# Optimization experiments

Hardware: AMD Instinct MI355X
Metric: run time of the kernel (lower is better)

The kernel has to match this reference:

```python
import jax, jax.numpy as jnp
import numpy as np

B, T, F = 4096, 72, 9
H = 64            # GRU units per direction
DENSE = 128
P = 24            # predict_window


def _gru_scan(xp, h0, U, br, act):
    """xp: (T,B,3H) precomputed input projections; Keras reset_after=True GRU."""
    def step(h, x_t):
        rec = h @ U + br                      # (B,3H)
        xz, xr, xh = jnp.split(x_t, 3, axis=-1)
        rz, rr, rh = jnp.split(rec, 3, axis=-1)
        z = jax.nn.sigmoid(xz + rz)
        r = jax.nn.sigmoid(xr + rr)
        hh = act(xh + r * rh)
        h_new = z * h + (1.0 - z) * hh
        return h_new, h_new
    hT, hs = jax.lax.scan(step, h0, xp)
    return hT, hs


def _bigru(x, h0f, h0b, Wf, Uf, bif, brf, Wb, Ub, bib, brb, act, return_sequences):
    xt = jnp.swapaxes(x, 0, 1)                # (T,B,F)
    xpf = xt @ Wf + bif                       # (T,B,3H)
    xpb = xt[::-1] @ Wb + bib                 # reversed time for backward dir
    hTf, hsf = _gru_scan(xpf, h0f, Uf, brf, act)
    hTb, hsb = _gru_scan(xpb, h0b, Ub, brb, act)
    if return_sequences:
        out = jnp.concatenate([hsf, hsb[::-1]], axis=-1)   # (T,B,2H)
        return jnp.swapaxes(out, 0, 1)                      # (B,T,2H)
    return jnp.concatenate([hTf, hTb], axis=-1)             # (B,2H)


def _glorot(key, shape):
    fan_in, fan_out = shape[0], shape[-1]
    lim = np.sqrt(6.0 / (fan_in + fan_out))
    return jax.random.uniform(key, shape, jnp.float32, -lim, lim)


def setup_inputs() -> dict:
    key = jax.random.key(0)
    ks = jax.random.split(key, 16)
    d = {
        "x": jax.random.normal(ks[0], (B, T, F), jnp.float32),
        "h0_fwd": jnp.zeros((B, H), jnp.float32),
        "h0_bwd": jnp.zeros((B, H), jnp.float32),
        # d1 (input F=9), forward & backward directions
        "d1f_W": _glorot(ks[1], (F, 3 * H)), "d1f_U": _glorot(ks[2], (H, 3 * H)),
        "d1f_bi": jnp.zeros((3 * H,), jnp.float32), "d1f_br": jnp.zeros((3 * H,), jnp.float32),
        "d1b_W": _glorot(ks[3], (F, 3 * H)), "d1b_U": _glorot(ks[4], (H, 3 * H)),
        "d1b_bi": jnp.zeros((3 * H,), jnp.float32), "d1b_br": jnp.zeros((3 * H,), jnp.float32),
        # d2 (input 2H=128)
        "d2f_W": _glorot(ks[5], (2 * H, 3 * H)), "d2f_U": _glorot(ks[6], (H, 3 * H)),
        "d2f_bi": jnp.zeros((3 * H,), jnp.float32), "d2f_br": jnp.zeros((3 * H,), jnp.float32),
        "d2b_W": _glorot(ks[7], (2 * H, 3 * H)), "d2b_U": _glorot(ks[8], (H, 3 * H)),
        "d2b_bi": jnp.zeros((3 * H,), jnp.float32), "d2b_br": jnp.zeros((3 * H,), jnp.float32),
        # dense heads
        "dense_W": _glorot(ks[9], (2 * H, DENSE)), "dense_b": jnp.zeros((DENSE,), jnp.float32),
        "out_W": _glorot(ks[10], (DENSE, P)), "out_b": jnp.zeros((P,), jnp.float32),
    }
    return d


def reference(x, h0_fwd, h0_bwd,
              d1f_W, d1f_U, d1f_bi, d1f_br, d1b_W, d1b_U, d1b_bi, d1b_br,
              d2f_W, d2f_U, d2f_bi, d2f_br, d2b_W, d2b_U, d2b_bi, d2b_br,
              dense_W, dense_b, out_W, out_b):
    # d1: Bidirectional GRU(64, activation=relu), return_sequences=True, initial_state=hidden
    seq = _bigru(x, h0_fwd, h0_bwd,
                 d1f_W, d1f_U, d1f_bi, d1f_br,
                 d1b_W, d1b_U, d1b_bi, d1b_br,
                 jax.nn.relu, True)                         # (B,T,128)
    # d2: Bidirectional GRU(64, activation=tanh), zero initial state, last-state output
    z0 = jnp.zeros((x.shape[0], H), seq.dtype)
    feat = _bigru(seq, z0, z0,
                  d2f_W, d2f_U, d2f_bi, d2f_br,
                  d2b_W, d2b_U, d2b_bi, d2b_br,
                  jnp.tanh, False)                          # (B,128)
    h = jax.nn.relu(feat @ dense_W + dense_b)               # (B,128)
    out = jax.nn.softmax(h @ out_W + out_b, axis=-1)        # (B,P)
    return out
```

## Files before the change

kernel.cpp:

```cpp
#include <hip/hip_runtime.h>
#include <hip/hip_bf16.h>

typedef __attribute__((ext_vector_type(8))) short short8;
typedef __attribute__((ext_vector_type(4))) float f32x4;
typedef float float4a __attribute__((ext_vector_type(4), aligned(4)));
typedef unsigned short ushort4u __attribute__((ext_vector_type(4), aligned(2)));
typedef unsigned short ush;

#define MFMA_B16(a, b, c) __builtin_amdgcn_mfma_f32_16x16x32_bf16((a), (b), (c), 0, 0, 0)

__device__ __forceinline__ float bf2f(ush u) {
    union { unsigned int i; float f; } v; v.i = ((unsigned int)u) << 16; return v.f;
}
__device__ __forceinline__ ush f2bf(float f) {
    union { float f; unsigned int i; } v; v.f = f;
    unsigned int r = v.i + 0x7fffu + ((v.i >> 16) & 1u);
    return (ush)(r >> 16);
}
__device__ __forceinline__ float rcp_f(float x) { return __builtin_amdgcn_rcpf(x); }
__device__ __forceinline__ float sigm_pre(float x) {
    return rcp_f(1.0f + __builtin_amdgcn_exp2f(x));
}
__device__ __forceinline__ float tanh_pre(float x) {
    return 1.0f - 2.0f * rcp_f(__builtin_amdgcn_exp2f(x) + 1.0f);
}

__device__ __forceinline__ void lds_barrier() {
    asm volatile("s_waitcnt lgkmcnt(0)" ::: "memory");
    __builtin_amdgcn_s_barrier();
    asm volatile("" ::: "memory");
}

__device__ __forceinline__ bool probe_bf16(const ush* p, int tid, int* s_cnt) {
    if (tid == 0) *s_cnt = 0;
    __syncthreads();
    ush s = p[tid & 255];
    int e = (s >> 7) & 0xFF;
    if (tid < 256 && e >= 117 && e <= 137) atomicAdd(s_cnt, 1);
    __syncthreads();
    return *s_cnt >= 200;
}

struct WArgs {
    const void* src[20];
    int off[21];
};

__global__ __launch_bounds__(256)
void convert_w(WArgs a, ush* __restrict__ arena, const ush* __restrict__ probe)
{
    __shared__ int cnt;
    const bool bf = probe_bf16(probe, threadIdx.x, &cnt);
    const int total = a.off[20];
    for (int i = blockIdx.x * 256 + threadIdx.x; i < total; i += gridDim.x * 256) {
        int t = 0;
        while (t < 19 && i >= a.off[t + 1]) ++t;
        const int local = i - a.off[t];
        float v = bf ? bf2f(((const ush*)a.src[t])[local])
                     : ((const float*)a.src[t])[local];
        if (t < 16) {
            const int col = local % 192;
            if (col < 128) v *= -1.4426950408889634f;
            else if (t >= 8) v *= 2.885390081777927f;
        }
        arena[i] = f2bf(v);
    }
}

struct XR { float4a f; ushort4u h; };

__device__ __forceinline__ XR loadx(const void* X, bool xbf, size_t row72, int tx, int q) {
    XR r;
    r.f = (float4a){0.f, 0.f, 0.f, 0.f};
    r.h = (ushort4u){0, 0, 0, 0};
    if (xbf) {
        const ush* p = (const ush*)X + (row72 + (size_t)tx) * 9 + q * 4;
        if (q < 2) r.h = *(const ushort4u*)p;
        else if (q == 2) r.h[0] = p[0];
    } else {
        const float* p = (const float*)X + (row72 + (size_t)tx) * 9 + q * 4;
        if (q < 2) r.f = *(const float4a*)p;
        else if (q == 2) r.f[0] = p[0];
    }
    return r;
}

__device__ __forceinline__ short8 convx(bool xbf, float4a rf, ushort4u rh) {
    short8 r;
    if (xbf) {
#pragma unroll
        for (int j = 0; j < 4; ++j) { r[2 * j] = (short)rh[j]; r[2 * j + 1] = 0; }
    } else {
#pragma unroll
        for (int j = 0; j < 4; ++j) {
            ush hi = f2bf(rf[j]);
            ush lo = f2bf(rf[j] - bf2f(hi));
            r[2 * j] = (short)hi; r[2 * j + 1] = (short)lo;
        }
    }
    return r;
}

__global__ __launch_bounds__(256, 1)
void gru1_kernel(const void* __restrict__ X, const void* __restrict__ h0f,
                 const void* __restrict__ h0b, int cb, int bchunk,
                 const ush* __restrict__ Wf, const ush* __restrict__ Uf,
                 const ush* __restrict__ bif, const ush* __restrict__ brf,
                 const ush* __restrict__ Wb, const ush* __restrict__ Ub,
                 const ush* __restrict__ bib, const ush* __restrict__ brb,
                 ush* __restrict__ seq)
{
    const int tid  = threadIdx.x;
    const int lane = tid & 63;
    const int wv   = tid >> 6;
    const int q    = lane >> 4;
    const int ln   = lane & 15;
    const int dir  = blockIdx.y;
    const int lb0  = blockIdx.x * 16;
    const int gb0  = cb + lb0;
    const int u    = wv * 16 + ln;

    const ush* W  = dir ? Wb  : Wf;
    const ush* U  = dir ? Ub  : Uf;
    const ush* bi = dir ? bib : bif;
    const ush* br = dir ? brb : brf;
    const void* h0 = dir ? h0b : h0f;

    __shared__ __align__(16) ush Ah[2][16][72];
    __shared__ int s_cnt;

    const bool xbf = probe_bf16((const ush*)X, tid, &s_cnt);

    short8 bU[3][2];
    short8 bW[3];
#pragma unroll
    for (int g = 0; g < 3; ++g) {
        const int col = g * 64 + u;
#pragma unroll
        for (int ks = 0; ks < 2; ++ks) {
            short8 f;
#pragma unroll
            for (int j = 0; j < 8; ++j) {
                int kp = ks * 32 + q * 8 + j;
                f[j] = (short)U[(size_t)kp * 192 + col];
            }
            bU[g][ks] = f;
        }
        short8 fw;
#pragma unroll
        for (int j = 0; j < 8; ++j) {
            int kp = q * 8 + j;
            fw[j] = (kp < 18) ? (short)W[(size_t)(kp >> 1) * 192 + col] : (short)0;
        }
        bW[g] = fw;
    }

    const float bz  = bf2f(bi[u])       + bf2f(br[u]);
    const float brg = bf2f(bi[64 + u])  + bf2f(br[64 + u]);
    const float bih = bf2f(bi[128 + u]);
    const float brh = bf2f(br[128 + u]);
    const f32x4 Cz  = {bz,  bz,  bz,  bz};
    const f32x4 Cr  = {brg, brg, brg, brg};
    const f32x4 Chx = {bih, bih, bih, bih};
    const f32x4 Chr = {brh, brh, brh, brh};

    float hreg[4];
#pragma unroll
    for (int i = 0; i < 4; ++i) {
        int m = q * 4 + i;
        size_t idx = (size_t)(gb0 + m) * 64 + u;
        float hv = xbf ? bf2f(((const ush*)h0)[idx])
                       : ((const float*)h0)[idx];
        hreg[i] = hv;
        Ah[0][m][u] = f2bf(hv);
    }

    const int r2 = tid >> 3, c2 = tid & 7;

    const size_t row72 = (size_t)(gb0 + ln) * 72;
    short8 axc;
    XR rn;
    {
        XR r0 = loadx(X, xbf, row72, dir ? 71 : 0, q);
        axc = convx(xbf, r0.f, r0.h);
        rn  = loadx(X, xbf, row72, dir ? 70 : 1, q);
    }
    __syncthreads();

#pragma unroll 2
    for (int t = 0; t < 72; ++t) {
        const int cur = t & 1, nb = cur ^ 1;

        XR rr;
        rr.f = (float4a){0.f, 0.f, 0.f, 0.f};
        rr.h = (ushort4u){0, 0, 0, 0};
        if (t < 70) rr = loadx(X, xbf, row72, dir ? 69 - t : t + 2, q);

        if (t > 0 && tid < 128) {
            const int tw = dir ? (71 - (t - 1)) : (t - 1);
            int4 v = *(const int4*)&Ah[cur][r2][c2 * 8];
            *(int4*)(seq + ((size_t)tw * bchunk + lb0 + r2) * 128 + dir * 64 + c2 * 8) = v;
        }

        const ush* ap = &Ah[cur][ln][0];
        short8 a0 = *(const short8*)(ap + q * 8);
        short8 a1 = *(const short8*)(ap + 32 + q * 8);
        f32x4 az  = MFMA_B16(axc, bW[0], Cz);
        az        = MFMA_B16(a0, bU[0][0], az);
        az        = MFMA_B16(a1, bU[0][1], az);
        f32x4 ar  = MFMA_B16(axc, bW[1], Cr);
        ar        = MFMA_B16(a0, bU[1][0], ar);
        ar        = MFMA_B16(a1, bU[1][1], ar);
        f32x4 ahx = MFMA_B16(axc, bW[2], Chx);
        f32x4 ahr = MFMA_B16(a0, bU[2][0], Chr);
        ahr       = MFMA_B16(a1, bU[2][1], ahr);

#pragma unroll
        for (int i = 0; i < 4; ++i) {
            const int m = q * 4 + i;
            float z = sigm_pre(az[i]);
            float r = sigm_pre(ar[i]);
            float pre = ahx[i] + r * ahr[i];
            float hh = fmaxf(pre, 0.0f);
            float hn = hh + z * (hreg[i] - hh);
            hreg[i] = hn;
            Ah[nb][m][u] = f2bf(hn);
        }

        axc = convx(xbf, rn.f, rn.h);
        rn = rr;
        lds_barrier();
    }

    if (tid < 128) {
        const int tw = dir ? 0 : 71;
        int4 v = *(const int4*)&Ah[0][r2][c2 * 8];
        *(int4*)(seq + ((size_t)tw * bchunk + lb0 + r2) * 128 + dir * 64 + c2 * 8) = v;
    }
}

__global__ __launch_bounds__(256, 1)
void gru2_kernel(const ush* __restrict__ seq, int cb, int bchunk,
                 const ush* __restrict__ W2f, const ush* __restrict__ U2f,
                 const ush* __restrict__ bi2f, const ush* __restrict__ br2f,
                 const ush* __restrict__ W2b, const ush* __restrict__ U2b,
                 const ush* __restrict__ bi2b, const ush* __restrict__ br2b,
                 float* __restrict__ feat)
{
    const int tid  = threadIdx.x;
    const int lane = tid & 63;
    const int wv   = tid >> 6;
    const int q    = lane >> 4;
    const int ln   = lane & 15;
    const int dir  = blockIdx.y;
    const int lb0  = blockIdx.x * 16;
    const int gb0  = cb + lb0;
    const int u    = wv * 16 + ln;

    const ush* W  = dir ? W2b  : W2f;
    const ush* U  = dir ? U2b  : U2f;
    const ush* bi = dir ? bi2b : bi2f;
    const ush* br = dir ? br2b : br2f;

    __shared__ __align__(16) ush Ah[2][16][72];

    {
        ush* p = &Ah[0][0][0];
        for (int i = tid; i < 16 * 72; i += 256) p[i] = 0;
    }

    const long long tstride = (long long)bchunk * 128 * (dir ? -1 : 1);
    const ush* sptr0 = seq + ((size_t)(lb0 + ln)) * 128 + q * 8
                     + (dir ? 71ll * bchunk * 128 : 0);

    short8 bU[3][2];
    short8 bV[3][4];
#pragma unroll
    for (int g = 0; g < 3; ++g) {
        const int col = g * 64 + u;
#pragma unroll
        for (int ks = 0; ks < 2; ++ks) {
            short8 f;
#pragma unroll
            for (int j = 0; j < 8; ++j) {
                int kp = ks * 32 + q * 8 + j;
                f[j] = (short)U[(size_t)kp * 192 + col];
            }
            bU[g][ks] = f;
        }
#pragma unroll
        for (int ks = 0; ks < 4; ++ks) {
            short8 fv;
#pragma unroll
            for (int j = 0; j < 8; ++j) {
                int kp = ks * 32 + q * 8 + j;
                fv[j] = (short)W[(size_t)kp * 192 + col];
            }
            bV[g][ks] = fv;
        }
    }

    const float bz  = bf2f(bi[u])       + bf2f(br[u]);
    const float brg = bf2f(bi[64 + u])  + bf2f(br[64 + u]);
    const float bih = bf2f(bi[128 + u]);
    const float brh = bf2f(br[128 + u]);
    const f32x4 Cz  = {bz,  bz,  bz,  bz};
    const f32x4 Cr  = {brg, brg, brg, brg};
    const f32x4 Chx = {bih, bih, bih, bih};
    const f32x4 Chr = {brh, brh, brh, brh};

    float hreg[4];
#pragma unroll
    for (int i = 0; i < 4; ++i) hreg[i] = 0.0f;

    f32x4 P0, P1, P2;
    {
        const ush* sp = sptr0;
        short8 s0 = *(const short8*)(sp);
        short8 s1 = *(const short8*)(sp + 32);
        short8 s2 = *(const short8*)(sp + 64);
        short8 s3 = *(const short8*)(sp + 96);
        P0 = MFMA_B16(s0, bV[0][0], Cz);
        P0 = MFMA_B16(s1, bV[0][1], P0);
        P0 = MFMA_B16(s2, bV[0][2], P0);
        P0 = MFMA_B16(s3, bV[0][3], P0);
        P1 = MFMA_B16(s0, bV[1][0], Cr);
        P1 = MFMA_B16(s1, bV[1][1], P1);
        P1 = MFMA_B16(s2, bV[1][2], P1);
        P1 = MFMA_B16(s3, bV[1][3], P1);
        P2 = MFMA_B16(s0, bV[2][0], Chx);
        P2 = MFMA_B16(s1, bV[2][1], P2);
        P2 = MFMA_B16(s2, bV[2][2], P2);
        P2 = MFMA_B16(s3, bV[2][3], P2);
    }
    short8 c0, c1, c2, c3, g0, g1, g2, g3;
    {
        const ush* sp = sptr0 + tstride;
        c0 = *(const short8*)(sp);
        c1 = *(const short8*)(sp + 32);
        c2 = *(const short8*)(sp + 64);
        c3 = *(const short8*)(sp + 96);
    }
    {
        const ush* sp = sptr0 + 2 * tstride;
        g0 = *(const short8*)(sp);
        g1 = *(const short8*)(sp + 32);
        g2 = *(const short8*)(sp + 64);
        g3 = *(const short8*)(sp + 96);
    }
    __syncthreads();

#pragma unroll 2
    for (int t = 0; t < 72; ++t) {
        const int cur = t & 1, nb = cur ^ 1;

        short8 f0 = g0, f1 = g1, f2 = g2, f3 = g3;
        if (t < 69) {
            const ush* sp = sptr0 + (long long)(t + 3) * tstride;
            f0 = *(const short8*)(sp);
            f1 = *(const short8*)(sp + 32);
            f2 = *(const short8*)(sp + 64);
            f3 = *(const short8*)(sp + 96);
        }

        const ush* ap = &Ah[cur][ln][0];
        short8 a0 = *(const short8*)(ap + q * 8);
        short8 a1 = *(const short8*)(ap + 32 + q * 8);
        f32x4 az  = MFMA_B16(a0, bU[0][0], P0);
        az        = MFMA_B16(a1, bU[0][1], az);
        f32x4 ar  = MFMA_B16(a0, bU[1][0], P1);
        ar        = MFMA_B16(a1, bU[1][1], ar);
        f32x4 ahr = MFMA_B16(a0, bU[2][0], Chr);
        ahr       = MFMA_B16(a1, bU[2][1], ahr);
        f32x4 ahx = P2;

#pragma unroll
        for (int i = 0; i < 4; ++i) {
            const int m = q * 4 + i;
            float z = sigm_pre(az[i]);
            float r = sigm_pre(ar[i]);
            float pre = ahx[i] + r * ahr[i];
            float hh = tanh_pre(pre);
            float hn = hh + z * (hreg[i] - hh);
            hreg[i] = hn;
            Ah[nb][m][u] = f2bf(hn);
        }

        if (t < 71) {
            P0 = MFMA_B16(c0, bV[0][0], Cz);
            P0 = MFMA_B16(c1, bV[0][1], P0);
            P0 = MFMA_B16(c2, bV[0][2], P0);
            P0 = MFMA_B16(c3, bV[0][3], P0);
            P1 = MFMA_B16(c0, bV[1][0], Cr);
            P1 = MFMA_B16(c1, bV[1][1], P1);
            P1 = MFMA_B16(c2, bV[1][2], P1);
            P1 = MFMA_B16(c3, bV[1][3], P1);
            P2 = MFMA_B16(c0, bV[2][0], Chx);
            P2 = MFMA_B16(c1, bV[2][1], P2);
            P2 = MFMA_B16(c2, bV[2][2], P2);
            P2 = MFMA_B16(c3, bV[2][3], P2);
        }
        c0 = g0; c1 = g1; c2 = g2; c3 = g3;
        g0 = f0; g1 = f1; g2 = f2; g3 = f3;
        lds_barrier();
    }

#pragma unroll
    for (int i = 0; i < 4; ++i) {
        const int m = q * 4 + i;
        feat[(size_t)(gb0 + m) * 128 + dir * 64 + u] = hreg[i];
    }
}

__global__ __launch_bounds__(256, 1)
void head_kernel(const float* __restrict__ feat,
                 const ush* __restrict__ dW, const ush* __restrict__ db,
                 const ush* __restrict__ oW, const ush* __restrict__ ob,
                 float* __restrict__ out)
{
    const int tid = threadIdx.x;
    const int b0  = blockIdx.x * 16;

    __shared__ __align__(16) ush Wl[128][136];
    __shared__ __align__(16) float fs[16][128];
    __shared__ __align__(16) float hs[16][136];
    __shared__ __align__(16) float ls[16][32];

    for (int i = tid; i < 2048; i += 256) {
        const int k = i >> 4;
        const int c = (i & 15) * 8;
        *(int4*)&Wl[k][c] = *(const int4*)(dW + (size_t)k * 128 + c);
    }
    {
        const float4* src = (const float4*)(feat + (size_t)b0 * 128);
        float4* dst = (float4*)&fs[0][0];
        for (int i = tid; i < 512; i += 256) dst[i] = src[i];
    }
    __syncthreads();

    {
        const int row = tid >> 4;
        const int j0  = (tid & 15) * 8;
        float acc[8];
#pragma unroll
        for (int jj = 0; jj < 8; ++jj) acc[jj] = bf2f(db[j0 + jj]);
        for (int k = 0; k < 128; ++k) {
            float f = fs[row][k];
            short8 w = *(const short8*)&Wl[k][j0];
#pragma unroll
            for (int jj = 0; jj < 8; ++jj)
                acc[jj] += f * bf2f((ush)w[jj]);
        }
#pragma unroll
        for (int jj = 0; jj < 8; ++jj) hs[row][j0 + jj] = fmaxf(acc[jj], 0.0f);
    }
    __syncthreads();

    for (int e = tid; e < 16 * 24; e += 256) {
        const int row = e / 24, l = e - 24 * row;
        float acc = bf2f(ob[l]);
        for (int k = 0; k < 128; ++k)
            acc += hs[row][k] * bf2f(oW[(size_t)k * 24 + l]);
        ls[row][l] = acc;
    }
    __syncthreads();

    for (int e = tid; e < 16 * 24; e += 256) {
        const int row = e / 24, l = e - 24 * row;
        float mx = ls[row][0];
#pragma unroll
        for (int k = 1; k < 24; ++k) mx = fmaxf(mx, ls[row][k]);
        float s = 0.0f;
#pragma unroll
        for (int k = 0; k < 24; ++k) s += __expf(ls[row][k] - mx);
        float v = __expf(ls[row][l] - mx) * rcp_f(s);
        out[(size_t)(b0 + row) * 24 + l] = v;
    }
}

extern "C" void kernel_launch(void* const* d_in, const int* in_sizes, int n_in,
                              void* d_out, int out_size, void* d_ws, size_t ws_size,
                              hipStream_t stream) {
    (void)in_sizes; (void)n_in; (void)out_size;

    static const int wc[20] = {
        1728, 12288, 192, 192,
        1728, 12288, 192, 192,
        24576, 12288, 192, 192,
        24576, 12288, 192, 192,
        16384, 128,
        3072, 24
    };

    WArgs a;
    int off = 0;
    for (int t = 0; t < 20; ++t) {
        a.src[t] = d_in[t + 3];
        a.off[t] = off;
        off += wc[t];
    }
    a.off[20] = off;

    const unsigned long long arena_bytes = 245952ull;
    const unsigned long long feat_bytes  = 4096ull * 128ull * 4ull;
    const unsigned long long seq_full    = 72ull * 4096ull * 128ull * 2ull;
    const unsigned long long fixed       = arena_bytes + feat_bytes;

    int nc = 32;
    for (int c = 1; c <= 32; c *= 2) {
        if (fixed + seq_full / (unsigned long long)c <= (unsigned long long)ws_size) { nc = c; break; }
    }
    const int bchunk = 4096 / nc;

    ush* arena  = (ush*)d_ws;
    float* feat = (float*)((char*)d_ws + arena_bytes);
    ush* seq    = (ush*)((char*)d_ws + fixed);

    convert_w<<<128, 256, 0, stream>>>(a, arena, (const ush*)d_in[0]);

    const ush* d1fW = arena + a.off[0];
    const ush* d1fU = arena + a.off[1];
    const ush* d1fbi= arena + a.off[2];
    const ush* d1fbr= arena + a.off[3];
    const ush* d1bW = arena + a.off[4];
    const ush* d1bU = arena + a.off[5];
    const ush* d1bbi= arena + a.off[6];
    const ush* d1bbr= arena + a.off[7];
    const ush* d2fW = arena + a.off[8];
    const ush* d2fU = arena + a.off[9];
    const ush* d2fbi= arena + a.off[10];
    const ush* d2fbr= arena + a.off[11];
    const ush* d2bW = arena + a.off[12];
    const ush* d2bU = arena + a.off[13];
    const ush* d2bbi= arena + a.off[14];
    const ush* d2bbr= arena + a.off[15];
    const ush* dW   = arena + a.off[16];
    const ush* db   = arena + a.off[17];
    const ush* oW   = arena + a.off[18];
    const ush* ob   = arena + a.off[19];

    for (int c = 0; c < nc; ++c) {
        const int cb = c * bchunk;
        gru1_kernel<<<dim3(bchunk / 16, 2), 256, 0, stream>>>(
            d_in[0], d_in[1], d_in[2], cb, bchunk,
            d1fW, d1fU, d1fbi, d1fbr, d1bW, d1bU, d1bbi, d1bbr, seq);
        gru2_kernel<<<dim3(bchunk / 16, 2), 256, 0, stream>>>(
            seq, cb, bchunk,
            d2fW, d2fU, d2fbi, d2fbr, d2bW, d2bU, d2bbi, d2bbr, feat);
    }
    head_kernel<<<256, 256, 0, stream>>>(
        feat, dW, db, oW, ob, (float*)d_out);
}
```

Baseline: 242.6 us.

## Warp-specialize gru2 into projection producers and recurrence consumers; stage gru1 inputs via LDS

gru2 now launches 512 threads. Four producer waves compute the input projections (seq @ W) one step ahead into a double-buffered LDS buffer, and four consumer waves run the recurrent MFMAs and gate math, so the projection work leaves the serial critical path. In gru1, per-lane vector loads of x plus in-register conversion are replaced by 144 threads that each load one scalar, split it into bf16 hi/lo, and write it to an LDS tile read by MFMA. This costs extra LDS traffic and barriers every step and doubles the thread count per block, which could hurt occupancy or lengthen each step.

```diff
diff --git a/kernel.cpp b/kernel.cpp
--- a/kernel.cpp
+++ b/kernel.cpp
@@ -3,8 +3,6 @@
 
 typedef __attribute__((ext_vector_type(8))) short short8;
 typedef __attribute__((ext_vector_type(4))) float f32x4;
-typedef float float4a __attribute__((ext_vector_type(4), aligned(4)));
-typedef unsigned short ushort4u __attribute__((ext_vector_type(4), aligned(2)));
 typedef unsigned short ush;
 
 #define MFMA_B16(a, b, c) __builtin_amdgcn_mfma_f32_16x16x32_bf16((a), (b), (c), 0, 0, 0)
@@ -65,40 +63,6 @@
         }
         arena[i] = f2bf(v);
     }
-}
-
-struct XR { float4a f; ushort4u h; };
-
-__device__ __forceinline__ XR loadx(const void* X, bool xbf, size_t row72, int tx, int q) {
-    XR r;
-    r.f = (float4a){0.f, 0.f, 0.f, 0.f};
-    r.h = (ushort4u){0, 0, 0, 0};
-    if (xbf) {
-        const ush* p = (const ush*)X + (row72 + (size_t)tx) * 9 + q * 4;
-        if (q < 2) r.h = *(const ushort4u*)p;
-        else if (q == 2) r.h[0] = p[0];
-    } else {
-        const float* p = (const float*)X + (row72 + (size_t)tx) * 9 + q * 4;
-        if (q < 2) r.f = *(const float4a*)p;
-        else if (q == 2) r.f[0] = p[0];
-    }
-    return r;
-}
-
-__device__ __forceinline__ short8 convx(bool xbf, float4a rf, ushort4u rh) {
-    short8 r;
-    if (xbf) {
-#pragma unroll
-        for (int j = 0; j < 4; ++j) { r[2 * j] = (short)rh[j]; r[2 * j + 1] = 0; }
-    } else {
-#pragma unroll
-        for (int j = 0; j < 4; ++j) {
-            ush hi = f2bf(rf[j]);
-            ush lo = f2bf(rf[j] - bf2f(hi));
-            r[2 * j] = (short)hi; r[2 * j + 1] = (short)lo;
-        }
-    }
-    return r;
 }
 
 __global__ __launch_bounds__(256, 1)
@@ -127,9 +91,29 @@
     const void* h0 = dir ? h0b : h0f;
 
     __shared__ __align__(16) ush Ah[2][16][72];
+    __shared__ __align__(16) ush Ax[2][16][40];
     __shared__ int s_cnt;
 
     const bool xbf = probe_bf16((const ush*)X, tid, &s_cnt);
+
+    {
+        ush* p = &Ax[0][0][0];
+        for (int i = tid; i < 2 * 16 * 40; i += 256) p[i] = 0;
+    }
+    __syncthreads();
+
+    {
+        const int tx0 = dir ? 71 : 0;
+        if (tid < 144) {
+            int r = tid / 9, k = tid - 9 * r;
+            size_t idx = ((size_t)(gb0 + r) * 72 + tx0) * 9 + k;
+            ush hv, lv;
+            if (xbf) { hv = ((const ush*)X)[idx]; lv = 0; }
+            else { float v = ((const float*)X)[idx]; hv = f2bf(v); lv = f2bf(v - bf2f(hv)); }
+            Ax[0][r][2 * k]     = hv;
+            Ax[0][r][2 * k + 1] = lv;
+        }
+    }
 
     short8 bU[3][2];
     short8 bW[3];
@@ -176,14 +160,14 @@
     }
 
     const int r2 = tid >> 3, c2 = tid & 7;
-
-    const size_t row72 = (size_t)(gb0 + ln) * 72;
-    short8 axc;
-    XR rn;
-    {
-        XR r0 = loadx(X, xbf, row72, dir ? 71 : 0, q);
-        axc = convx(xbf, r0.f, r0.h);
-        rn  = loadx(X, xbf, row72, dir ? 70 : 1, q);
+    const int r0x = tid / 9, k0x = tid - 9 * r0x;
+
+    unsigned int craw = 0;
+    if (tid < 144) {
+        const int tx = dir ? 70 : 1;
+        size_t idx = ((size_t)(gb0 + r0x) * 72 + tx) * 9 + k0x;
+        craw = xbf ? (unsigned int)((const ush*)X)[idx]
+                   : ((const unsigned int*)X)[idx];
     }
     __syncthreads();
 
@@ -191,10 +175,13 @@
     for (int t = 0; t < 72; ++t) {
         const int cur = t & 1, nb = cur ^ 1;
 
-        XR rr;
-        rr.f = (float4a){0.f, 0.f, 0.f, 0.f};
-        rr.h = (ushort4u){0, 0, 0, 0};
-        if (t < 70) rr = loadx(X, xbf, row72, dir ? 69 - t : t + 2, q);
+        unsigned int fraw = 0;
+        if (t < 70 && tid < 144) {
+            const int tx = dir ? (69 - t) : (t + 2);
+            size_t idx = ((size_t)(gb0 + r0x) * 72 + tx) * 9 + k0x;
+            fraw = xbf ? (unsigned int)((const ush*)X)[idx]
+                       : ((const unsigned int*)X)[idx];
+        }
 
         if (t > 0 && tid < 128) {
             const int tw = dir ? (71 - (t - 1)) : (t - 1);
@@ -205,13 +192,14 @@
         const ush* ap = &Ah[cur][ln][0];
         short8 a0 = *(const short8*)(ap + q * 8);
         short8 a1 = *(const short8*)(ap + 32 + q * 8);
-        f32x4 az  = MFMA_B16(axc, bW[0], Cz);
+        short8 ax = *(const short8*)(&Ax[cur][ln][q * 8]);
+        f32x4 az  = MFMA_B16(ax, bW[0], Cz);
         az        = MFMA_B16(a0, bU[0][0], az);
         az        = MFMA_B16(a1, bU[0][1], az);
-        f32x4 ar  = MFMA_B16(axc, bW[1], Cr);
+        f32x4 ar  = MFMA_B16(ax, bW[1], Cr);
         ar        = MFMA_B16(a0, bU[1][0], ar);
         ar        = MFMA_B16(a1, bU[1][1], ar);
-        f32x4 ahx = MFMA_B16(axc, bW[2], Chx);
+        f32x4 ahx = MFMA_B16(ax, bW[2], Chx);
         f32x4 ahr = MFMA_B16(a0, bU[2][0], Chr);
         ahr       = MFMA_B16(a1, bU[2][1], ahr);
 
@@ -227,8 +215,17 @@
             Ah[nb][m][u] = f2bf(hn);
         }
 
-        axc = convx(xbf, rn.f, rn.h);
-        rn = rr;
+        if (t < 71 && tid < 144) {
+            ush hv, lv;
+            if (xbf) { hv = (ush)craw; lv = 0; }
+            else {
+                float v = __uint_as_float(craw);
+                hv = f2bf(v); lv = f2bf(v - bf2f(hv));
+            }
+            Ax[nb][r0x][2 * k0x]     = hv;
+            Ax[nb][r0x][2 * k0x + 1] = lv;
+        }
+        craw = fraw;
         lds_barrier();
     }
 
@@ -239,7 +236,35 @@
     }
 }
 
-__global__ __launch_bounds__(256, 1)
+#define PCOMPUTE(E, BUFI)                                                      \
+    do {                                                                       \
+        f32x4 p0 = MFMA_B16(E##0, bV[0][0], Cg0);                              \
+        p0 = MFMA_B16(E##1, bV[0][1], p0);                                     \
+        p0 = MFMA_B16(E##2, bV[0][2], p0);                                     \
+        p0 = MFMA_B16(E##3, bV[0][3], p0);                                     \
+        *(f32x4*)&Pbuf[BUFI][0][pn][poff] = p0;                                \
+        f32x4 p1 = MFMA_B16(E##0, bV[1][0], Cg1);                              \
+        p1 = MFMA_B16(E##1, bV[1][1], p1);                                     \
+        p1 = MFMA_B16(E##2, bV[1][2], p1);                                     \
+        p1 = MFMA_B16(E##3, bV[1][3], p1);                                     \
+        *(f32x4*)&Pbuf[BUFI][1][pn][poff] = p1;                                \
+        f32x4 p2 = MFMA_B16(E##0, bV[2][0], Cg2);                              \
+        p2 = MFMA_B16(E##1, bV[2][1], p2);                                     \
+        p2 = MFMA_B16(E##2, bV[2][2], p2);                                     \
+        p2 = MFMA_B16(E##3, bV[2][3], p2);                                     \
+        *(f32x4*)&Pbuf[BUFI][2][pn][poff] = p2;                                \
+    } while (0)
+
+#define ELOAD(E, T)                                                            \
+    do {                                                                       \
+        const ush* sp_ = sptr0 + (long long)(T) * tstride;                     \
+        E##0 = *(const short8*)(sp_);                                          \
+        E##1 = *(const short8*)(sp_ + 32);                                     \
+        E##2 = *(const short8*)(sp_ + 64);                                     \
+        E##3 = *(const short8*)(sp_ + 96);                                     \
+    } while (0)
+
+__global__ __launch_bounds__(512, 1)
 void gru2_kernel(const ush* __restrict__ seq, int cb, int bchunk,
                  const ush* __restrict__ W2f, const ush* __restrict__ U2f,
                  const ush* __restrict__ bi2f, const ush* __restrict__ br2f,
@@ -248,167 +273,134 @@
                  float* __restrict__ feat)
 {
     const int tid  = threadIdx.x;
+    const int wv   = tid >> 6;
     const int lane = tid & 63;
-    const int wv   = tid >> 6;
     const int q    = lane >> 4;
     const int ln   = lane & 15;
     const int dir  = blockIdx.y;
     const int lb0  = blockIdx.x * 16;
     const int gb0  = cb + lb0;
-    const int u    = wv * 16 + ln;
 
     const ush* W  = dir ? W2b  : W2f;
     const ush* U  = dir ? U2b  : U2f;
     const ush* bi = dir ? bi2b : bi2f;
     const ush* br = dir ? br2b : br2f;
 
+    __shared__ __align__(16) float Pbuf[2][3][4][288];
     __shared__ __align__(16) ush Ah[2][16][72];
 
-    {
-        ush* p = &Ah[0][0][0];
-        for (int i = tid; i < 16 * 72; i += 256) p[i] = 0;
-    }
-
-    const long long tstride = (long long)bchunk * 128 * (dir ? -1 : 1);
-    const ush* sptr0 = seq + ((size_t)(lb0 + ln)) * 128 + q * 8
-                     + (dir ? 71ll * bchunk * 128 : 0);
-
-    short8 bU[3][2];
-    short8 bV[3][4];
-#pragma unroll
-    for (int g = 0; g < 3; ++g) {
-        const int col = g * 64 + u;
-#pragma unroll
-        for (int ks = 0; ks < 2; ++ks) {
-            short8 f;
-#pragma unroll
-            for (int j = 0; j < 8; ++j) {
-                int kp = ks * 32 + q * 8 + j;
-                f[j] = (short)U[(size_t)kp * 192 + col];
+    const int poff = (lane >> 3) * 36 + (lane & 7) * 4;
+
+    if (wv < 4) {
+        const int pn = wv;
+        const int u2 = pn * 16 + ln;
+
+        short8 bV[3][4];
+#pragma unroll
+        for (int g = 0; g < 3; ++g) {
+            const int col = g * 64 + u2;
+#pragma unroll
+            for (int ks = 0; ks < 4; ++ks) {
+                short8 f;
+#pragma unroll
+                for (int j = 0; j < 8; ++j) {
+                    int kp = ks * 32 + q * 8 + j;
+                    f[j] = (short)W[(size_t)kp * 192 + col];
+                }
+                bV[g][ks] = f;
             }
-            bU[g][ks] = f;
-        }
-#pragma unroll
-        for (int ks = 0; ks < 4; ++ks) {
-            short8 fv;
-#pragma unroll
-            for (int j = 0; j < 8; ++j) {
-                int kp = ks * 32 + q * 8 + j;
-                fv[j] = (short)W[(size_t)kp * 192 + col];
+        }
+        const float bz  = bf2f(bi[u2]) + bf2f(br[u2]);
+        const float brg = bf2f(bi[64 + u2]) + bf2f(br[64 + u2]);
+        const float bih = bf2f(bi[128 + u2]);
+        const f32x4 Cg0 = {bz, bz, bz, bz};
+        const f32x4 Cg1 = {brg, brg, brg, brg};
+        const f32x4 Cg2 = {bih, bih, bih, bih};
+
+        const long long tstride = (long long)bchunk * 128 * (dir ? -1 : 1);
+        const ush* sptr0 = seq + (size_t)(lb0 + ln) * 128 + q * 8
+                         + (dir ? 71ll * bchunk * 128 : 0);
+
+        short8 EA0, EA1, EA2, EA3, EB0, EB1, EB2, EB3;
+        ELOAD(EA, 0);
+        PCOMPUTE(EA, 0);
+        ELOAD(EA, 1);
+        ELOAD(EB, 2);
+        lds_barrier();
+
+        for (int t = 0; t < 72; t += 2) {
+            PCOMPUTE(EA, 1);
+            if (t <= 68) ELOAD(EA, t + 3);
+            lds_barrier();
+            if (t + 1 < 71) PCOMPUTE(EB, 0);
+            if (t + 1 <= 68) ELOAD(EB, t + 4);
+            lds_barrier();
+        }
+    } else {
+        const int cn = wv - 4;
+        const int u2 = cn * 16 + ln;
+
+        short8 bU[3][2];
+#pragma unroll
+        for (int g = 0; g < 3; ++g) {
+            const int col = g * 64 + u2;
+#pragma unroll
+            for (int ks = 0; ks < 2; ++ks) {
+                short8 f;
+#pragma unroll
+                for (int j = 0; j < 8; ++j) {
+                    int kp = ks * 32 + q * 8 + j;
+                    f[j] = (short)U[(size_t)kp * 192 + col];
+                }
+                bU[g][ks] = f;
             }
-            bV[g][ks] = fv;
-        }
-    }
-
-    const float bz  = bf2f(bi[u])       + bf2f(br[u]);
-    const float brg = bf2f(bi[64 + u])  + bf2f(br[64 + u]);
-    const float bih = bf2f(bi[128 + u]);
-    const float brh = bf2f(br[128 + u]);
-    const f32x4 Cz  = {bz,  bz,  bz,  bz};
-    const f32x4 Cr  = {brg, brg, brg, brg};
-    const f32x4 Chx = {bih, bih, bih, bih};
-    const f32x4 Chr = {brh, brh, brh, brh};
-
-    float hreg[4];
-#pragma unroll
-    for (int i = 0; i < 4; ++i) hreg[i] = 0.0f;
-
-    f32x4 P0, P1, P2;
-    {
-        const ush* sp = sptr0;
-        short8 s0 = *(const short8*)(sp);
-        short8 s1 = *(const short8*)(sp + 32);
-        short8 s2 = *(const short8*)(sp + 64);
-        short8 s3 = *(const short8*)(sp + 96);
-        P0 = MFMA_B16(s0, bV[0][0], Cz);
-        P0 = MFMA_B16(s1, bV[0][1], P0);
-        P0 = MFMA_B16(s2, bV[0][2], P0);
-        P0 = MFMA_B16(s3, bV[0][3], P0);
-        P1 = MFMA_B16(s0, bV[1][0], Cr);
-        P1 = MFMA_B16(s1, bV[1][1], P1);
-        P1 = MFMA_B16(s2, bV[1][2], P1);
-        P1 = MFMA_B16(s3, bV[1][3], P1);
-        P2 = MFMA_B16(s0, bV[2][0], Chx);
-        P2 = MFMA_B16(s1, bV[2][1], P2);
-        P2 = MFMA_B16(s2, bV[2][2], P2);
-        P2 = MFMA_B16(s3, bV[2][3], P2);
-    }
-    short8 c0, c1, c2, c3, g0, g1, g2, g3;
-    {
-        const ush* sp = sptr0 + tstride;
-        c0 = *(const short8*)(sp);
-        c1 = *(const short8*)(sp + 32);
-        c2 = *(const short8*)(sp + 64);
-        c3 = *(const short8*)(sp + 96);
-    }
-    {
-        const ush* sp = sptr0 + 2 * tstride;
-        g0 = *(const short8*)(sp);
-        g1 = *(const short8*)(sp + 32);
-        g2 = *(const short8*)(sp + 64);
-        g3 = *(const short8*)(sp + 96);
-    }
-    __syncthreads();
-
-#pragma unroll 2
-    for (int t = 0; t < 72; ++t) {
-        const int cur = t & 1, nb = cur ^ 1;
-
-        short8 f0 = g0, f1 = g1, f2 = g2, f3 = g3;
-        if (t < 69) {
-            const ush* sp = sptr0 + (long long)(t + 3) * tstride;
-            f0 = *(const short8*)(sp);
-            f1 = *(const short8*)(sp + 32);
-            f2 = *(const short8*)(sp + 64);
-            f3 = *(const short8*)(sp + 96);
-        }
-
-        const ush* ap = &Ah[cur][ln][0];
-        short8 a0 = *(const short8*)(ap + q * 8);
-        short8 a1 = *(const short8*)(ap + 32 + q * 8);
-        f32x4 az  = MFMA_B16(a0, bU[0][0], P0);
-        az        = MFMA_B16(a1, bU[0][1], az);
-        f32x4 ar  = MFMA_B16(a0, bU[1][0], P1);
-        ar        = MFMA_B16(a1, bU[1][1], ar);
-        f32x4 ahr = MFMA_B16(a0, bU[2][0], Chr);
-        ahr       = MFMA_B16(a1, bU[2][1], ahr);
-        f32x4 ahx = P2;
+        }
+        const float brh = bf2f(br[128 + u2]);
+        const f32x4 Chr = {brh, brh, brh, brh};
+
+        for (int i = tid - 256; i < 16 * 72; i += 256) (&Ah[0][0][0])[i] = 0;
+        float hreg[4];
+#pragma unroll
+        for (int i = 0; i < 4; ++i) hreg[i] = 0.0f;
+        lds_barrier();
+
+        for (int t = 0; t < 72; ++t) {
+            const int cur = t & 1, nb = cur ^ 1;
+
+            f32x4 Pz = *(const f32x4*)&Pbuf[cur][0][cn][poff];
+            f32x4 Pr = *(const f32x4*)&Pbuf[cur][1][cn][poff];
+            f32x4 Pc = *(const f32x4*)&Pbuf[cur][2][cn][poff];
+
+            const ush* ap = &Ah[cur][ln][0];
+            short8 a0 = *(const short8*)(ap + q * 8);
+            short8 a1 = *(const short8*)(ap + 32 + q * 8);
+
+            f32x4 az  = MFMA_B16(a0, bU[0][0], Pz);
+            az        = MFMA_B16(a1, bU[0][1], az);
+            f32x4 ar  = MFMA_B16(a0, bU[1][0], Pr);
+            ar        = MFMA_B16(a1, bU[1][1], ar);
+            f32x4 ahr = MFMA_B16(a0, bU[2][0], Chr);
+            ahr       = MFMA_B16(a1, bU[2][1], ahr);
+
+#pragma unroll
+            for (int i = 0; i < 4; ++i) {
+                const int m = q * 4 + i;
+                float z = sigm_pre(az[i]);
+                float r = sigm_pre(ar[i]);
+                float pre = Pc[i] + r * ahr[i];
+                float hh = tanh_pre(pre);
+                float hn = hh + z * (hreg[i] - hh);
+                hreg[i] = hn;
+                Ah[nb][m][u2] = f2bf(hn);
+            }
+            lds_barrier();
+        }
 
 #pragma unroll
         for (int i = 0; i < 4; ++i) {
             const int m = q * 4 + i;
-            float z = sigm_pre(az[i]);
-            float r = sigm_pre(ar[i]);
-            float pre = ahx[i] + r * ahr[i];
-            float hh = tanh_pre(pre);
-            float hn = hh + z * (hreg[i] - hh);
-            hreg[i] = hn;
-            Ah[nb][m][u] = f2bf(hn);
-        }
-
-        if (t < 71) {
-            P0 = MFMA_B16(c0, bV[0][0], Cz);
-            P0 = MFMA_B16(c1, bV[0][1], P0);
-            P0 = MFMA_B16(c2, bV[0][2], P0);
-            P0 = MFMA_B16(c3, bV[0][3], P0);
-            P1 = MFMA_B16(c0, bV[1][0], Cr);
-            P1 = MFMA_B16(c1, bV[1][1], P1);
-            P1 = MFMA_B16(c2, bV[1][2], P1);
-            P1 = MFMA_B16(c3, bV[1][3], P1);
-            P2 = MFMA_B16(c0, bV[2][0], Chx);
-            P2 = MFMA_B16(c1, bV[2][1], P2);
-            P2 = MFMA_B16(c2, bV[2][2], P2);
-            P2 = MFMA_B16(c3, bV[2][3], P2);
-        }
-        c0 = g0; c1 = g1; c2 = g2; c3 = g3;
-        g0 = f0; g1 = f1; g2 = f2; g3 = f3;
-        lds_barrier();
-    }
-
-#pragma unroll
-    for (int i = 0; i < 4; ++i) {
-        const int m = q * 4 + i;
-        feat[(size_t)(gb0 + m) * 128 + dir * 64 + u] = hreg[i];
+            feat[(size_t)(gb0 + m) * 128 + dir * 64 + u2] = hreg[i];
+        }
     }
 }
 
@@ -544,7 +536,7 @@
         gru1_kernel<<<dim3(bchunk / 16, 2), 256, 0, stream>>>(
             d_in[0], d_in[1], d_in[2], cb, bchunk,
             d1fW, d1fU, d1fbi, d1fbr, d1bW, d1bU, d1bbi, d1bbr, seq);
-        gru2_kernel<<<dim3(bchunk / 16, 2), 256, 0, stream>>>(
+        gru2_kernel<<<dim3(bchunk / 16, 2), 512, 0, stream>>>(
             seq, cb, bchunk,
             d2fW, d2fU, d2fbi, d2fbr, d2bW, d2bU, d2bbi, d2bbr, feat);
     }
```

New measurement: 242.6 us. No clear change (-0.0%).
